# Performance work log

Measured on AMD Instinct MI355X. Metric: run time of the kernel, lower is better.

## Reference

```python
import jax, jax.numpy as jnp
import numpy as np

TAU = 0.08


def setup_inputs() -> dict:
    key = jax.random.key(0)
    k1, k2 = jax.random.split(key)
    pos_waves = jax.random.normal(k1, (32, 64, 8192), dtype=jnp.float32)
    neg_waves = jax.random.normal(k2, (32, 64, 8192), dtype=jnp.float32)
    return {"pos_waves": pos_waves, "neg_waves": neg_waves}


def _normalize(w):
    # global min/max over the whole wave tensor (matches torch.min/torch.max on 2D tensor)
    lo = jnp.min(w, axis=(1, 2), keepdims=True)  # [N,1,1]
    hi = jnp.max(w, axis=(1, 2), keepdims=True)
    return (w - lo) / (hi - lo)


def _pairwise_negpearson(X, Y):
    # X: [N,B,T], Y: [M,B,T] -> mean over B of (1 - pearson) for every (n,m) pair
    T = X.shape[-1]
    sx = jnp.sum(X, axis=-1)            # [N,B]
    sy = jnp.sum(Y, axis=-1)            # [M,B]
    sx2 = jnp.sum(X * X, axis=-1)       # [N,B]
    sy2 = jnp.sum(Y * Y, axis=-1)       # [M,B]
    sxy = jnp.einsum('nbt,mbt->nmb', X, Y)  # [N,M,B]
    num = T * sxy - sx[:, None, :] * sy[None, :, :]
    den = jnp.sqrt((T * sx2 - sx * sx)[:, None, :] * (T * sy2 - sy * sy)[None, :, :])
    return jnp.mean(1.0 - num / den, axis=-1)  # [N,M]


def reference(pos_waves, neg_waves):
    P = _normalize(pos_waves)   # [N,B,T]
    Q = _normalize(neg_waves)   # [M,B,T]
    N = P.shape[0]

    d_pp = _pairwise_negpearson(P, P)                    # [N,N]
    upper = jnp.triu(jnp.ones((N, N), dtype=bool), k=1)  # i < j pairs only
    pos_total = jnp.sum(jnp.where(upper, jnp.exp(d_pp / TAU), 0.0))

    d_pn = _pairwise_negpearson(P, Q)                    # [N,M]
    neg_total = jnp.sum(jnp.exp(d_pn / TAU))

    return jnp.log10(pos_total / neg_total + 1.0)
```

## Files before the change

kernel.cpp:

```cpp
#include <hip/hip_runtime.h>
#include <cmath>

#define N_ 32
#define B_ 64
#define T_ 8192
#define CPB 16
#define PSTRIDE 2176
#define PADH 264

typedef _Float16 half4 __attribute__((ext_vector_type(4)));
typedef _Float16 half8 __attribute__((ext_vector_type(8)));
typedef float floatx16 __attribute__((ext_vector_type(16)));

__global__ __launch_bounds__(256, 4) void k_stage1(const float* __restrict__ pos,
                                                   const float* __restrict__ neg,
                                                   float* __restrict__ partial) {
    __shared__ __align__(16) char smem[2 * 32 * PADH * 2];
    _Float16(*tile)[32][PADH] = (_Float16(*)[32][PADH])smem;
    float* scratch = (float*)smem;

    const int bid = blockIdx.x;
    const int b = bid >> 4, c = bid & 15;
    const int tid = threadIdx.x;
    const int w = tid >> 6, lane = tid & 63;
    const int row = tid >> 3;
    const int oct = tid & 7;
    const int m = lane & 31, h = lane >> 5;

    const float* xrow = pos + ((long)row * B_ + b) * T_ + c * 512;
    const float* yrow = neg + ((long)row * B_ + b) * T_ + c * 512;

    floatx16 accpp = {};
    floatx16 accpn = {};
    float sx = 0.f, sx2 = 0.f, sy = 0.f, sy2 = 0.f;

#pragma unroll
    for (int s = 0; s < 2; ++s) {
        __syncthreads();
        const float4* px = (const float4*)(xrow + s * 256);
        const float4* py = (const float4*)(yrow + s * 256);
#pragma unroll
        for (int f = 0; f < 8; ++f) {
            float4 v = px[f * 8 + oct];
            sx += v.x + v.y + v.z + v.w;
            sx2 = fmaf(v.x, v.x, sx2); sx2 = fmaf(v.y, v.y, sx2);
            sx2 = fmaf(v.z, v.z, sx2); sx2 = fmaf(v.w, v.w, sx2);
            half4 hv = {(_Float16)v.x, (_Float16)v.y, (_Float16)v.z, (_Float16)v.w};
            *(half4*)&tile[0][row][f * 32 + oct * 4] = hv;

            float4 u = py[f * 8 + oct];
            sy += u.x + u.y + u.z + u.w;
            sy2 = fmaf(u.x, u.x, sy2); sy2 = fmaf(u.y, u.y, sy2);
            sy2 = fmaf(u.z, u.z, sy2); sy2 = fmaf(u.w, u.w, sy2);
            half4 hu = {(_Float16)u.x, (_Float16)u.y, (_Float16)u.z, (_Float16)u.w};
            *(half4*)&tile[1][row][f * 32 + oct * 4] = hu;
        }
        __syncthreads();
#pragma unroll
        for (int kk = 0; kk < 4; ++kk) {
            const int t0 = w * 64 + kk * 16 + h * 8;
            half8 xf = *(const half8*)&tile[0][m][t0];
            half8 yf = *(const half8*)&tile[1][m][t0];
            accpp = __builtin_amdgcn_mfma_f32_32x32x16_f16(xf, xf, accpp, 0, 0, 0);
            accpn = __builtin_amdgcn_mfma_f32_32x32x16_f16(xf, yf, accpn, 0, 0, 0);
        }
    }

    sx += __shfl_xor(sx, 1); sx += __shfl_xor(sx, 2); sx += __shfl_xor(sx, 4);
    sx2 += __shfl_xor(sx2, 1); sx2 += __shfl_xor(sx2, 2); sx2 += __shfl_xor(sx2, 4);
    sy += __shfl_xor(sy, 1); sy += __shfl_xor(sy, 2); sy += __shfl_xor(sy, 4);
    sy2 += __shfl_xor(sy2, 1); sy2 += __shfl_xor(sy2, 2); sy2 += __shfl_xor(sy2, 4);

    float* out = partial + (long)bid * PSTRIDE;
    if (oct < 4) {
        float v = (oct == 0) ? sx : (oct == 1) ? sx2 : (oct == 2) ? sy : sy2;
        out[2048 + oct * 32 + row] = v;
    }

    __syncthreads();
#pragma unroll
    for (int reg = 0; reg < 16; ++reg) {
        int rr = (reg & 3) + 8 * (reg >> 2) + 4 * h;
        scratch[w * 2048 + rr * 32 + m] = accpp[reg];
        scratch[w * 2048 + 1024 + rr * 32 + m] = accpn[reg];
    }
    __syncthreads();
    for (int o = tid; o < 2048; o += 256)
        out[o] = scratch[o] + scratch[2048 + o] + scratch[4096 + o] + scratch[6144 + o];
}

__global__ void k_reduce(const float* __restrict__ partial, float* __restrict__ red) {
    const int b = blockIdx.y;
    const int o = blockIdx.x * 128 + threadIdx.x;
    const float* in = partial + (long)b * CPB * PSTRIDE;
    float s = 0.f;
#pragma unroll
    for (int c = 0; c < CPB; ++c) s += in[c * PSTRIDE + o];
    red[(long)b * PSTRIDE + o] = s;
}

__global__ void k_entries(const float* __restrict__ red, double* __restrict__ blocksums) {
    const int tid = threadIdx.x;
    const int w = tid >> 6, lane = tid & 63;
    const int entry = blockIdx.x * 4 + w;
    const int mat = entry >> 10;
    const int idx = entry & 1023;
    const int n = idx >> 5, m = idx & 31;

    const float* rb = red + (long)lane * PSTRIDE;
    float g = rb[mat * 1024 + idx];
    float sxn = rb[2048 + n];
    float sx2n = rb[2080 + n];
    float sym, sy2m;
    if (mat == 0) {
        sym = rb[2048 + m];
        sy2m = rb[2080 + m];
    } else {
        sym = rb[2112 + m];
        sy2m = rb[2144 + m];
    }

    double num = (double)T_ * (double)g - (double)sxn * (double)sym;
    double vx = (double)T_ * (double)sx2n - (double)sxn * (double)sxn;
    double vy = (double)T_ * (double)sy2m - (double)sym * (double)sym;
    double contrib = 1.0 - num / sqrt(vx * vy);

#pragma unroll
    for (int off = 32; off; off >>= 1) contrib += __shfl_down(contrib, off);

    __shared__ double s_pos[4], s_neg[4];
    if (lane == 0) {
        double d = contrib * (1.0 / B_);
        double term = exp(d / 0.08);
        double p = 0.0, q = 0.0;
        if (mat == 0) {
            if (n < m) p = term;
        } else {
            q = term;
        }
        s_pos[w] = p;
        s_neg[w] = q;
    }
    __syncthreads();
    if (tid == 0) {
        blocksums[blockIdx.x * 2 + 0] = s_pos[0] + s_pos[1] + s_pos[2] + s_pos[3];
        blocksums[blockIdx.x * 2 + 1] = s_neg[0] + s_neg[1] + s_neg[2] + s_neg[3];
    }
}

__global__ void k_final(const double* __restrict__ blocksums, float* __restrict__ out) {
    __shared__ double sp[256], sn[256];
    const int tid = threadIdx.x;
    double p = 0.0, q = 0.0;
    for (int i = tid; i < 512; i += 256) {
        p += blocksums[2 * i + 0];
        q += blocksums[2 * i + 1];
    }
    sp[tid] = p;
    sn[tid] = q;
    __syncthreads();
    for (int s = 128; s; s >>= 1) {
        if (tid < s) {
            sp[tid] += sp[tid + s];
            sn[tid] += sn[tid + s];
        }
        __syncthreads();
    }
    if (tid == 0) out[0] = (float)log10(sp[0] / sn[0] + 1.0);
}

extern "C" void kernel_launch(void* const* d_in, const int* in_sizes, int n_in,
                              void* d_out, int out_size, void* d_ws, size_t ws_size,
                              hipStream_t stream) {
    const float* pos = (const float*)d_in[0];
    const float* neg = (const float*)d_in[1];
    float* out = (float*)d_out;

    char* ws = (char*)d_ws;
    float* partial = (float*)ws;
    float* red = (float*)(ws + (size_t)1024 * PSTRIDE * 4);
    double* blocksums = (double*)(ws + (size_t)1024 * PSTRIDE * 4 + (size_t)64 * PSTRIDE * 4);

    k_stage1<<<1024, 256, 0, stream>>>(pos, neg, partial);
    k_reduce<<<dim3(17, 64), 128, 0, stream>>>(partial, red);
    k_entries<<<512, 256, 0, stream>>>(red, blocksums);
    k_final<<<1, 256, 0, stream>>>(blocksums, out);
}
```

Baseline: 156.8 us.

## Split MFMA work across 8 waves by output quadrant, drop LDS split-K reduction

Stage 1 now runs 512 threads per block. Each of 8 waves computes one 16x16 quadrant of either the PP or PN Gram matrix over the full 256-wide time tile using 16x16x32 MFMAs, instead of 4 waves each doing a split-K 32x32 slice. Results are written directly to global, which removes the LDS scratch round trip, the cross-wave sum and a barrier. Global loads are also batched ahead of the conversions to expose more memory parallelism. In exchange, each wave now issues more LDS reads relative to MFMA work.

```diff
diff --git a/kernel.cpp b/kernel.cpp
--- a/kernel.cpp
+++ b/kernel.cpp
@@ -10,28 +10,27 @@
 
 typedef _Float16 half4 __attribute__((ext_vector_type(4)));
 typedef _Float16 half8 __attribute__((ext_vector_type(8)));
-typedef float floatx16 __attribute__((ext_vector_type(16)));
+typedef float floatx4 __attribute__((ext_vector_type(4)));
 
-__global__ __launch_bounds__(256, 4) void k_stage1(const float* __restrict__ pos,
+__global__ __launch_bounds__(512, 8) void k_stage1(const float* __restrict__ pos,
                                                    const float* __restrict__ neg,
                                                    float* __restrict__ partial) {
-    __shared__ __align__(16) char smem[2 * 32 * PADH * 2];
-    _Float16(*tile)[32][PADH] = (_Float16(*)[32][PADH])smem;
-    float* scratch = (float*)smem;
+    __shared__ _Float16 tile[2][32][PADH];
 
     const int bid = blockIdx.x;
     const int b = bid >> 4, c = bid & 15;
     const int tid = threadIdx.x;
-    const int w = tid >> 6, lane = tid & 63;
-    const int row = tid >> 3;
-    const int oct = tid & 7;
-    const int m = lane & 31, h = lane >> 5;
+    const int wave = tid >> 6, lane = tid & 63;
+    const int row = tid >> 4;
+    const int idx = tid & 15;
+    const int mat = wave >> 2;
+    const int qi = (wave >> 1) & 1, qj = wave & 1;
+    const int m16 = lane & 15, h2 = lane >> 4;
 
     const float* xrow = pos + ((long)row * B_ + b) * T_ + c * 512;
     const float* yrow = neg + ((long)row * B_ + b) * T_ + c * 512;
 
-    floatx16 accpp = {};
-    floatx16 accpn = {};
+    floatx4 acc = {};
     float sx = 0.f, sx2 = 0.f, sy = 0.f, sy2 = 0.f;
 
 #pragma unroll
@@ -39,54 +38,64 @@
         __syncthreads();
         const float4* px = (const float4*)(xrow + s * 256);
         const float4* py = (const float4*)(yrow + s * 256);
+
+        float4 vx[4], vy[4];
 #pragma unroll
-        for (int f = 0; f < 8; ++f) {
-            float4 v = px[f * 8 + oct];
+        for (int f = 0; f < 4; ++f) vx[f] = px[f * 16 + idx];
+#pragma unroll
+        for (int f = 0; f < 4; ++f) vy[f] = py[f * 16 + idx];
+#pragma unroll
+        for (int f = 0; f < 4; ++f) {
+            float4 v = vx[f];
             sx += v.x + v.y + v.z + v.w;
             sx2 = fmaf(v.x, v.x, sx2); sx2 = fmaf(v.y, v.y, sx2);
             sx2 = fmaf(v.z, v.z, sx2); sx2 = fmaf(v.w, v.w, sx2);
             half4 hv = {(_Float16)v.x, (_Float16)v.y, (_Float16)v.z, (_Float16)v.w};
-            *(half4*)&tile[0][row][f * 32 + oct * 4] = hv;
-
-            float4 u = py[f * 8 + oct];
+            *(half4*)&tile[0][row][(f * 16 + idx) * 4] = hv;
+        }
+#pragma unroll
+        for (int f = 0; f < 4; ++f) {
+            float4 u = vy[f];
             sy += u.x + u.y + u.z + u.w;
             sy2 = fmaf(u.x, u.x, sy2); sy2 = fmaf(u.y, u.y, sy2);
             sy2 = fmaf(u.z, u.z, sy2); sy2 = fmaf(u.w, u.w, sy2);
             half4 hu = {(_Float16)u.x, (_Float16)u.y, (_Float16)u.z, (_Float16)u.w};
-            *(half4*)&tile[1][row][f * 32 + oct * 4] = hu;
+            *(half4*)&tile[1][row][(f * 16 + idx) * 4] = hu;
         }
         __syncthreads();
+
+        const _Float16* abase = &tile[0][qi * 16 + m16][h2 * 8];
+        const _Float16* bbase = &tile[mat][qj * 16 + m16][h2 * 8];
 #pragma unroll
-        for (int kk = 0; kk < 4; ++kk) {
-            const int t0 = w * 64 + kk * 16 + h * 8;
-            half8 xf = *(const half8*)&tile[0][m][t0];
-            half8 yf = *(const half8*)&tile[1][m][t0];
-            accpp = __builtin_amdgcn_mfma_f32_32x32x16_f16(xf, xf, accpp, 0, 0, 0);
-            accpn = __builtin_amdgcn_mfma_f32_32x32x16_f16(xf, yf, accpn, 0, 0, 0);
+        for (int k = 0; k < 8; ++k) {
+            half8 af = *(const half8*)(abase + k * 32);
+            half8 bf = *(const half8*)(bbase + k * 32);
+            acc = __builtin_amdgcn_mfma_f32_16x16x32_f16(af, bf, acc, 0, 0, 0);
         }
     }
 
-    sx += __shfl_xor(sx, 1); sx += __shfl_xor(sx, 2); sx += __shfl_xor(sx, 4);
-    sx2 += __shfl_xor(sx2, 1); sx2 += __shfl_xor(sx2, 2); sx2 += __shfl_xor(sx2, 4);
-    sy += __shfl_xor(sy, 1); sy += __shfl_xor(sy, 2); sy += __shfl_xor(sy, 4);
-    sy2 += __shfl_xor(sy2, 1); sy2 += __shfl_xor(sy2, 2); sy2 += __shfl_xor(sy2, 4);
+    sx += __shfl_xor(sx, 1); sx += __shfl_xor(sx, 2);
+    sx += __shfl_xor(sx, 4); sx += __shfl_xor(sx, 8);
+    sx2 += __shfl_xor(sx2, 1); sx2 += __shfl_xor(sx2, 2);
+    sx2 += __shfl_xor(sx2, 4); sx2 += __shfl_xor(sx2, 8);
+    sy += __shfl_xor(sy, 1); sy += __shfl_xor(sy, 2);
+    sy += __shfl_xor(sy, 4); sy += __shfl_xor(sy, 8);
+    sy2 += __shfl_xor(sy2, 1); sy2 += __shfl_xor(sy2, 2);
+    sy2 += __shfl_xor(sy2, 4); sy2 += __shfl_xor(sy2, 8);
 
     float* out = partial + (long)bid * PSTRIDE;
-    if (oct < 4) {
-        float v = (oct == 0) ? sx : (oct == 1) ? sx2 : (oct == 2) ? sy : sy2;
-        out[2048 + oct * 32 + row] = v;
+    if ((tid & 15) < 4) {
+        int kind = tid & 3;
+        float v = (kind == 0) ? sx : (kind == 1) ? sx2 : (kind == 2) ? sy : sy2;
+        out[2048 + kind * 32 + row] = v;
     }
 
-    __syncthreads();
 #pragma unroll
-    for (int reg = 0; reg < 16; ++reg) {
-        int rr = (reg & 3) + 8 * (reg >> 2) + 4 * h;
-        scratch[w * 2048 + rr * 32 + m] = accpp[reg];
-        scratch[w * 2048 + 1024 + rr * 32 + m] = accpn[reg];
+    for (int reg = 0; reg < 4; ++reg) {
+        int rr = qi * 16 + h2 * 4 + reg;
+        int cc = qj * 16 + m16;
+        out[mat * 1024 + rr * 32 + cc] = acc[reg];
     }
-    __syncthreads();
-    for (int o = tid; o < 2048; o += 256)
-        out[o] = scratch[o] + scratch[2048 + o] + scratch[4096 + o] + scratch[6144 + o];
 }
 
 __global__ void k_reduce(const float* __restrict__ partial, float* __restrict__ red) {
@@ -181,7 +190,7 @@
     float* red = (float*)(ws + (size_t)1024 * PSTRIDE * 4);
     double* blocksums = (double*)(ws + (size_t)1024 * PSTRIDE * 4 + (size_t)64 * PSTRIDE * 4);
 
-    k_stage1<<<1024, 256, 0, stream>>>(pos, neg, partial);
+    k_stage1<<<1024, 512, 0, stream>>>(pos, neg, partial);
     k_reduce<<<dim3(17, 64), 128, 0, stream>>>(partial, red);
     k_entries<<<512, 256, 0, stream>>>(red, blocksums);
     k_final<<<1, 256, 0, stream>>>(blocksums, out);
```

Result: no change. 154.1 us (-1.7%).
